# Performance work log

Measured on AMD Instinct MI355X. Metric: run time of the kernel, lower is better.

Reference implementation:

```python
import jax, jax.numpy as jnp
import numpy as np

B, T, U, V = 8, 128, 100, 1024
BLANK = 0
NEG = -1e30  # safe -inf surrogate (finite grads through logaddexp)


def setup_inputs() -> dict:
    key = jax.random.key(0)
    k1, k2 = jax.random.split(key)
    logits = jax.random.normal(k1, (B, T, U + 1, V), dtype=jnp.float32)
    # targets drawn from non-blank ids [1, V)
    targets = jax.random.randint(k2, (B, U), 1, V, dtype=jnp.int32)
    logit_lengths = jnp.full((B,), T, dtype=jnp.int32)
    target_lengths = jnp.full((B,), U, dtype=jnp.int32)
    return {"logits": logits, "targets": targets,
            "logit_lengths": logit_lengths, "target_lengths": target_lengths}


def _rnnt_nll(log_probs, targets, t_len, u_len):
    """Negative log-likelihood of one utterance.
    log_probs: [T, U+1, V] (log-softmaxed joiner output), targets: [U] int.
    alpha[t,u] = logaddexp(alpha[t-1,u] + blank[t-1,u], alpha[t,u-1] + emit[t,u-1]).
    """
    blank_lp = log_probs[:, :, BLANK]                      # [T, U+1]
    emit_lp = log_probs[:, jnp.arange(U), targets]         # [T, U]

    # row t=0: pure emissions
    alpha0 = jnp.concatenate([jnp.zeros((1,), log_probs.dtype),
                              jnp.cumsum(emit_lp[0])])     # [U+1]

    def combine(x, y):
        # linear log-space recurrence x[u] = logaddexp(c[u], x[u-1] + a[u])
        a1, c1 = x
        a2, c2 = y
        return (a1 + a2, jnp.logaddexp(c2, c1 + a2))

    def step(prev_row, inp):
        blank_prev, emit_t = inp                           # [U+1], [U]
        c = prev_row + blank_prev                          # vertical (blank) moves
        a = jnp.concatenate([jnp.full((1,), NEG, log_probs.dtype), emit_t])
        _, row = jax.lax.associative_scan(combine, (a, c))
        return row, row

    _, rows = jax.lax.scan(step, alpha0, (blank_lp[:-1], emit_lp[1:]))
    alpha = jnp.concatenate([alpha0[None, :], rows], axis=0)  # [T, U+1]

    ll = alpha[t_len - 1, u_len] + blank_lp[t_len - 1, u_len]
    return -ll


def reference(logits, targets, logit_lengths, target_lengths):
    log_probs = jax.nn.log_softmax(logits, axis=-1)
    # module passes src_lengths - 1 to rnnt_loss
    t_lens = logit_lengths - 1
    nll = jax.vmap(_rnnt_nll)(log_probs, targets, t_lens, target_lengths)
    return jnp.mean(nll)  # reduction='mean'
```

## Files before the change

kernel.cpp:

```cpp
#include <hip/hip_runtime.h>
#include <hip/hip_bf16.h>


constexpr int Bb = 8;
constexpr int Tt = 128;
constexpr int Uu = 100;
constexpr int Vv = 1024;
constexpr int UP1 = Uu + 1;
constexpr int DROWS = 244;
constexpr int DPAD  = 104;
constexpr int LROWS = 233;
constexpr int REG   = 29;
constexpr int NREG  = 8;

__device__ __forceinline__ unsigned short f2bf(float f) {
    unsigned int u = __builtin_bit_cast(unsigned int, f);
    u += 0x7fffu + ((u >> 16) & 1u);
    return (unsigned short)(u >> 16);
}
__device__ __forceinline__ float bflo(unsigned int p) {
    return __builtin_bit_cast(float, p << 16);
}
__device__ __forceinline__ float bfhi(unsigned int p) {
    return __builtin_bit_cast(float, p & 0xffff0000u);
}
__device__ __forceinline__ __hip_bfloat162 u2bf(unsigned int p) {
    __hip_bfloat162 h;
    __builtin_memcpy(&h, &p, sizeof(h));
    return h;
}
__device__ __forceinline__ unsigned int bf2u(__hip_bfloat162 h) {
    unsigned int p;
    __builtin_memcpy(&p, &h, sizeof(p));
    return p;
}

__device__ __forceinline__ unsigned int shr1u(unsigned int x) {
    return (unsigned int)__builtin_amdgcn_update_dpp(
        0, (int)x, 0x138, 0xf, 0xf, true);
}

__device__ __forceinline__ float readlane_f(float x, int lane) {
    return __builtin_bit_cast(float,
        __builtin_amdgcn_readlane(__builtin_bit_cast(int, x), lane));
}
__device__ __forceinline__ unsigned int readlane_u(unsigned int x, int lane) {
    return (unsigned int)__builtin_amdgcn_readlane((int)x, lane);
}

#define DPP_MAXSTEP(x, ctrl, rmask) {                                        \
    float _t = __builtin_bit_cast(float, __builtin_amdgcn_update_dpp(        \
        __builtin_bit_cast(int, x), __builtin_bit_cast(int, x),              \
        ctrl, rmask, 0xf, false));                                           \
    x = fmaxf(x, _t); }
#define WAVE_SCAN_MAX(x)           \
    DPP_MAXSTEP(x, 0x111, 0xf);    \
    DPP_MAXSTEP(x, 0x112, 0xf);    \
    DPP_MAXSTEP(x, 0x114, 0xf);    \
    DPP_MAXSTEP(x, 0x118, 0xf);    \
    DPP_MAXSTEP(x, 0x142, 0xa);    \
    DPP_MAXSTEP(x, 0x143, 0xc)

__global__ __launch_bounds__(256) void lse_kernel(
        const float* __restrict__ logits,
        const int*   __restrict__ targets,
        unsigned short* __restrict__ bS,
        unsigned short* __restrict__ eS,
        int* __restrict__ dcnt) {
    if (blockIdx.x == 0 && threadIdx.x == 0)
        __hip_atomic_store(dcnt, 0, __ATOMIC_RELAXED, __HIP_MEMORY_SCOPE_AGENT);

    const int wid  = blockIdx.x * 4 + (threadIdx.x >> 6);
    const int lane = threadIdx.x & 63;
    const int b   = wid / (Tt * UP1);
    const int rem = wid - b * (Tt * UP1);
    const int t   = rem / UP1;
    const int u   = rem - t * UP1;

    const float* row = logits + (size_t)wid * Vv;
    const float4* r4 = (const float4*)row;
    float4 x0 = r4[lane];
    float4 x1 = r4[lane + 64];
    float4 x2 = r4[lane + 128];
    float4 x3 = r4[lane + 192];

    float m = fmaxf(fmaxf(fmaxf(x0.x, x0.y), fmaxf(x0.z, x0.w)),
                    fmaxf(fmaxf(x1.x, x1.y), fmaxf(x1.z, x1.w)));
    m = fmaxf(m, fmaxf(fmaxf(fmaxf(x2.x, x2.y), fmaxf(x2.z, x2.w)),
                       fmaxf(fmaxf(x3.x, x3.y), fmaxf(x3.z, x3.w))));
    #pragma unroll
    for (int d = 32; d > 0; d >>= 1) m = fmaxf(m, __shfl_xor(m, d, 64));

    float s = __expf(x0.x - m) + __expf(x0.y - m) + __expf(x0.z - m) + __expf(x0.w - m)
            + __expf(x1.x - m) + __expf(x1.y - m) + __expf(x1.z - m) + __expf(x1.w - m)
            + __expf(x2.x - m) + __expf(x2.y - m) + __expf(x2.z - m) + __expf(x2.w - m)
            + __expf(x3.x - m) + __expf(x3.y - m) + __expf(x3.z - m) + __expf(x3.w - m);
    #pragma unroll
    for (int d = 32; d > 0; d >>= 1) s += __shfl_xor(s, d, 64);

    float lse = m + __logf(s);

    if (lane == 0) {
        const int dw = t + u + 1;
        bS[((size_t)b * DROWS + dw) * DPAD + u] = f2bf(__expf(x0.x - lse));
        if (u < Uu) {
            int tgt = targets[b * Uu + u];
            eS[((size_t)b * DROWS + dw) * DPAD + (u + 1)] = f2bf(__expf(row[tgt] - lse));
        }
    }
}

__global__ __launch_bounds__(576) void dp_kernel(
        const unsigned short* __restrict__ bS,
        const unsigned short* __restrict__ eS,
        const int* __restrict__ logit_lengths,
        const int* __restrict__ target_lengths,
        float* __restrict__ nll,
        int*   __restrict__ dcnt,
        float* __restrict__ out) {
    const int b    = blockIdx.x;
    const int tid  = threadIdx.x;
    const int wvi  = tid >> 6;
    const int lane = tid & 63;

    __shared__ __align__(16) unsigned short lB[LROWS][DPAD];
    __shared__ __align__(16) unsigned short lE[LROWS][DPAD];
    __shared__ int sflag[NREG];

    if (tid < NREG) sflag[tid] = 0;
    __syncthreads();

    const size_t bstride = (size_t)DROWS * DPAD;

    if (wvi >= 1) {
        const int w = wvi - 1;
        const int row0 = 1 + REG * w;
        constexpr int RBYTES = REG * DPAD * 2;
        const char* gb = (const char*)(bS + (size_t)b * bstride + (size_t)row0 * DPAD);
        const char* ge = (const char*)(eS + (size_t)b * bstride + (size_t)row0 * DPAD);
        char* db = (char*)&lB[row0][0];
        char* de = (char*)&lE[row0][0];
        for (int k = lane * 16; k < RBYTES; k += 64 * 16) {
            *(uint4*)(db + k) = *(const uint4*)(gb + k);
            *(uint4*)(de + k) = *(const uint4*)(ge + k);
        }
        if (lane < REG) {
            const int d = row0 + lane;
            lB[d][101] = 0; lB[d][102] = 0; lB[d][103] = 0;
            lE[d][0] = 0; lE[d][101] = 0; lE[d][102] = 0; lE[d][103] = 0;
        }
        __hip_atomic_store(&sflag[w], 1, __ATOMIC_RELEASE,
                           __HIP_MEMORY_SCOPE_WORKGROUP);
        return;
    }

    const int tl = logit_lengths[b];
    const int ul = target_lengths[b];
    const int t_idx = tl - 2;
    const int dcap  = t_idx + ul;

    const int u0 = lane * 2;

    unsigned int Pu = (lane == 0) ? 0x00003F80u : 0u;
    float S  = 0.0f;
    unsigned int capPu = (dcap == 0) ? 0x00003F80u : 0u;
    float capS = 0.0f;

#define PSTEP(dv, ubv, uev) do {                                       \
        unsigned int shP = shr1u(Pu);                                  \
        unsigned int M = __builtin_amdgcn_alignbit(Pu, shP, 16);       \
        Pu = bf2u(__hfma2(u2bf(ubv), u2bf(Pu),                         \
                          __hmul2(u2bf(uev), u2bf(M))));               \
        if ((dv) == dcap) { capPu = Pu; capS = S; }                    \
    } while (0)

#define RESCALE do {                                                   \
        float p0 = bflo(Pu), p1 = bfhi(Pu);                            \
        float gm = fmaxf(p0, p1);                                      \
        WAVE_SCAN_MAX(gm);                                             \
        float mm = fmaxf(readlane_f(gm, 63), 1e-30f);                  \
        float rr = 1.0f / mm;                                          \
        unsigned short rh = f2bf(rr);                                  \
        unsigned int rp = ((unsigned int)rh << 16) | rh;               \
        Pu = bf2u(__hmul2(u2bf(Pu), u2bf(rp)));                        \
        S += __logf(mm);                                               \
    } while (0)

#define LOADG(UB, UE, k) do {                                          \
        _Pragma("unroll")                                              \
        for (int r = 0; r < 8; ++r) {                                  \
            UB[r] = *(const unsigned int*)&lB[(k) * 8 + 1 + r][u0];    \
            UE[r] = *(const unsigned int*)&lE[(k) * 8 + 1 + r][u0];    \
        }                                                              \
    } while (0)

#define COMPG(UB, UE, k) do {                                          \
        _Pragma("unroll")                                              \
        for (int r = 0; r < 8; ++r)                                    \
            PSTEP((k) * 8 + 1 + r, UB[r], UE[r]);                      \
        RESCALE;                                                       \
    } while (0)

    int wcur = -1;
#define ENSURE(wn) do {                                                \
        while (wcur < (wn)) {                                          \
            ++wcur;                                                    \
            while (__hip_atomic_load(&sflag[wcur], __ATOMIC_ACQUIRE,   \
                       __HIP_MEMORY_SCOPE_WORKGROUP) == 0)             \
                __builtin_amdgcn_s_sleep(1);                           \
        }                                                              \
    } while (0)

    unsigned int Ab[8], Ae[8], Bb_[8], Be_[8];
    ENSURE(7 / REG);
    LOADG(Ab, Ae, 0);
    for (int c = 0; c < 14; ++c) {
        const int k0 = 2 * c, k1 = 2 * c + 1;
        ENSURE((8 * k1 + 7) / REG);
        LOADG(Bb_, Be_, k1);
        COMPG(Ab, Ae, k0);
        if (k1 < 28) {
            ENSURE((8 * (k1 + 1) + 7) / REG);
            LOADG(Ab, Ae, k1 + 1);
        }
        COMPG(Bb_, Be_, k1);
    }
    COMPG(Ab, Ae, 28);
#undef PSTEP
#undef RESCALE
#undef LOADG
#undef COMPG
#undef ENSURE

    unsigned int cw = readlane_u(capPu, ul >> 1);
    float capv = (ul & 1) ? bfhi(cw) : bflo(cw);

    if (lane == 0) {
        float blk = __builtin_bit_cast(float, ((unsigned int)lB[dcap + 1][ul]) << 16);
        float ll = __logf(capv) + capS + __logf(blk);
        __hip_atomic_store(&nll[b], -ll, __ATOMIC_RELEASE,
                           __HIP_MEMORY_SCOPE_AGENT);
        int prev = __hip_atomic_fetch_add(dcnt, 1, __ATOMIC_ACQ_REL,
                                          __HIP_MEMORY_SCOPE_AGENT);
        if (prev == Bb - 1) {
            float s = 0.0f;
            for (int i = 0; i < Bb; ++i)
                s += __hip_atomic_load(&nll[i], __ATOMIC_ACQUIRE,
                                       __HIP_MEMORY_SCOPE_AGENT);
            out[0] = s / (float)Bb;
        }
    }
}

extern "C" void kernel_launch(void* const* d_in, const int* in_sizes, int n_in,
                              void* d_out, int out_size, void* d_ws, size_t ws_size,
                              hipStream_t stream) {
    const float* logits         = (const float*)d_in[0];
    const int*   targets        = (const int*)d_in[1];
    const int*   logit_lengths  = (const int*)d_in[2];
    const int*   target_lengths = (const int*)d_in[3];
    float* out = (float*)d_out;

    int* dcnt = (int*)d_ws;
    unsigned short* bS = (unsigned short*)d_ws + 8;
    unsigned short* eS = bS + (size_t)Bb * DROWS * DPAD;
    float* nll = (float*)(eS + (size_t)Bb * DROWS * DPAD);

    const int rows = Bb * Tt * UP1;
    lse_kernel<<<rows / 4, 256, 0, stream>>>(logits, targets, bS, eS, dcnt);
    dp_kernel<<<Bb, 576, 0, stream>>>(bS, eS, logit_lengths, target_lengths,
                                      nll, dcnt, out);
}
```

Before: 97.06 us.

## Interleave blank/emit probabilities and run DP recurrence in fp32

Blank and emit probabilities now share one interleaved array, stored as pairs of (blank, emit) bf16 values per two columns, so each DP lane fetches both with one 8-byte LDS read. The staging waves use fully unrolled 16-byte copies with all loads issued before the stores. The anti-diagonal recurrence now keeps its state in fp32 registers with fma instead of packed bf16 arithmetic, which removes bf16 rounding from the accumulated state but roughly doubles the ALU ops per step on the serial critical path. The boundary zeroing is rewritten to match the new layout.

After: 88.81 us. 8.5% less time.

```diff
diff --git a/kernel.cpp b/kernel.cpp
--- a/kernel.cpp
+++ b/kernel.cpp
@@ -1,5 +1,4 @@
 #include <hip/hip_runtime.h>
-#include <hip/hip_bf16.h>
 
 
 constexpr int Bb = 8;
@@ -8,10 +7,12 @@
 constexpr int Vv = 1024;
 constexpr int UP1 = Uu + 1;
 constexpr int DROWS = 244;
-constexpr int DPAD  = 104;
+constexpr int PAIRS = 52;
+constexpr int ROWB  = PAIRS * 8;
 constexpr int LROWS = 233;
 constexpr int REG   = 29;
 constexpr int NREG  = 8;
+constexpr int RBYTES = REG * ROWB;
 
 __device__ __forceinline__ unsigned short f2bf(float f) {
     unsigned int u = __builtin_bit_cast(unsigned int, f);
@@ -24,28 +25,14 @@
 __device__ __forceinline__ float bfhi(unsigned int p) {
     return __builtin_bit_cast(float, p & 0xffff0000u);
 }
-__device__ __forceinline__ __hip_bfloat162 u2bf(unsigned int p) {
-    __hip_bfloat162 h;
-    __builtin_memcpy(&h, &p, sizeof(h));
-    return h;
-}
-__device__ __forceinline__ unsigned int bf2u(__hip_bfloat162 h) {
-    unsigned int p;
-    __builtin_memcpy(&p, &h, sizeof(p));
-    return p;
-}
-
-__device__ __forceinline__ unsigned int shr1u(unsigned int x) {
-    return (unsigned int)__builtin_amdgcn_update_dpp(
-        0, (int)x, 0x138, 0xf, 0xf, true);
-}
-
+
+__device__ __forceinline__ float wave_shr1(float x) {
+    return __builtin_bit_cast(float, __builtin_amdgcn_update_dpp(
+        0, __builtin_bit_cast(int, x), 0x138, 0xf, 0xf, true));
+}
 __device__ __forceinline__ float readlane_f(float x, int lane) {
     return __builtin_bit_cast(float,
         __builtin_amdgcn_readlane(__builtin_bit_cast(int, x), lane));
-}
-__device__ __forceinline__ unsigned int readlane_u(unsigned int x, int lane) {
-    return (unsigned int)__builtin_amdgcn_readlane((int)x, lane);
 }
 
 #define DPP_MAXSTEP(x, ctrl, rmask) {                                        \
@@ -64,8 +51,7 @@
 __global__ __launch_bounds__(256) void lse_kernel(
         const float* __restrict__ logits,
         const int*   __restrict__ targets,
-        unsigned short* __restrict__ bS,
-        unsigned short* __restrict__ eS,
+        unsigned short* __restrict__ gS,
         int* __restrict__ dcnt) {
     if (blockIdx.x == 0 && threadIdx.x == 0)
         __hip_atomic_store(dcnt, 0, __ATOMIC_RELAXED, __HIP_MEMORY_SCOPE_AGENT);
@@ -102,17 +88,18 @@
 
     if (lane == 0) {
         const int dw = t + u + 1;
-        bS[((size_t)b * DROWS + dw) * DPAD + u] = f2bf(__expf(x0.x - lse));
+        const size_t rowoff = ((size_t)b * DROWS + dw) * (PAIRS * 4);
+        gS[rowoff + (u >> 1) * 4 + (u & 1)] = f2bf(__expf(x0.x - lse));
         if (u < Uu) {
             int tgt = targets[b * Uu + u];
-            eS[((size_t)b * DROWS + dw) * DPAD + (u + 1)] = f2bf(__expf(row[tgt] - lse));
+            const int sidx = u + 1;
+            gS[rowoff + (sidx >> 1) * 4 + 2 + (sidx & 1)] = f2bf(__expf(row[tgt] - lse));
         }
     }
 }
 
 __global__ __launch_bounds__(576) void dp_kernel(
-        const unsigned short* __restrict__ bS,
-        const unsigned short* __restrict__ eS,
+        const unsigned short* __restrict__ gS,
         const int* __restrict__ logit_lengths,
         const int* __restrict__ target_lengths,
         float* __restrict__ nll,
@@ -123,31 +110,35 @@
     const int wvi  = tid >> 6;
     const int lane = tid & 63;
 
-    __shared__ __align__(16) unsigned short lB[LROWS][DPAD];
-    __shared__ __align__(16) unsigned short lE[LROWS][DPAD];
+    __shared__ __align__(16) unsigned short lBE[LROWS][PAIRS][4];
     __shared__ int sflag[NREG];
 
     if (tid < NREG) sflag[tid] = 0;
     __syncthreads();
-
-    const size_t bstride = (size_t)DROWS * DPAD;
 
     if (wvi >= 1) {
         const int w = wvi - 1;
         const int row0 = 1 + REG * w;
-        constexpr int RBYTES = REG * DPAD * 2;
-        const char* gb = (const char*)(bS + (size_t)b * bstride + (size_t)row0 * DPAD);
-        const char* ge = (const char*)(eS + (size_t)b * bstride + (size_t)row0 * DPAD);
-        char* db = (char*)&lB[row0][0];
-        char* de = (char*)&lE[row0][0];
-        for (int k = lane * 16; k < RBYTES; k += 64 * 16) {
-            *(uint4*)(db + k) = *(const uint4*)(gb + k);
-            *(uint4*)(de + k) = *(const uint4*)(ge + k);
-        }
+        const char* gb = (const char*)gS + ((size_t)b * DROWS + row0) * ROWB;
+        char* db = (char*)lBE + (size_t)row0 * ROWB;
+
+        uint4 v[12];
+        #pragma unroll
+        for (int i = 0; i < 12; ++i)
+            v[i] = *(const uint4*)(gb + lane * 16 + i * 1024);
+        #pragma unroll
+        for (int i = 0; i < 11; ++i)
+            *(uint4*)(db + lane * 16 + i * 1024) = v[i];
+        if (lane < 50)
+            *(uint4*)(db + lane * 16 + 11 * 1024) = v[11];
+
         if (lane < REG) {
             const int d = row0 + lane;
-            lB[d][101] = 0; lB[d][102] = 0; lB[d][103] = 0;
-            lE[d][0] = 0; lE[d][101] = 0; lE[d][102] = 0; lE[d][103] = 0;
+            lBE[d][0][2]  = 0;
+            lBE[d][50][1] = 0;
+            lBE[d][50][3] = 0;
+            lBE[d][51][0] = 0; lBE[d][51][1] = 0;
+            lBE[d][51][2] = 0; lBE[d][51][3] = 0;
         }
         __hip_atomic_store(&sflag[w], 1, __ATOMIC_RELEASE,
                            __HIP_MEMORY_SCOPE_WORKGROUP);
@@ -159,38 +150,39 @@
     const int t_idx = tl - 2;
     const int dcap  = t_idx + ul;
 
-    const int u0 = lane * 2;
-
-    unsigned int Pu = (lane == 0) ? 0x00003F80u : 0u;
+    const int lpair = (lane < 51) ? lane : 51;
+    const char* lbase = (const char*)lBE + lpair * 8;
+
+    float P0 = (lane == 0) ? 1.0f : 0.0f;
+    float P1 = 0.0f;
     float S  = 0.0f;
-    unsigned int capPu = (dcap == 0) ? 0x00003F80u : 0u;
-    float capS = 0.0f;
-
-#define PSTEP(dv, ubv, uev) do {                                       \
-        unsigned int shP = shr1u(Pu);                                  \
-        unsigned int M = __builtin_amdgcn_alignbit(Pu, shP, 16);       \
-        Pu = bf2u(__hfma2(u2bf(ubv), u2bf(Pu),                         \
-                          __hmul2(u2bf(uev), u2bf(M))));               \
-        if ((dv) == dcap) { capPu = Pu; capS = S; }                    \
+    float capP0 = (dcap == 0) ? 1.0f : 0.0f, capP1 = 0.0f, capS = 0.0f;
+
+#define PSTEP(dv, w0, w1) do {                                         \
+        float Bx = bflo(w0), By = bfhi(w0);                            \
+        float Ex = bflo(w1), Ey = bfhi(w1);                            \
+        float sh = wave_shr1(P1);                                      \
+        float n1 = fmaf(P1, By, P0 * Ey);                              \
+        float n0 = fmaf(P0, Bx, sh * Ex);                              \
+        P0 = n0; P1 = n1;                                              \
+        if ((dv) == dcap) { capP0 = n0; capP1 = n1; capS = S; }        \
     } while (0)
 
 #define RESCALE do {                                                   \
-        float p0 = bflo(Pu), p1 = bfhi(Pu);                            \
-        float gm = fmaxf(p0, p1);                                      \
+        float gm = fmaxf(P0, P1);                                      \
         WAVE_SCAN_MAX(gm);                                             \
         float mm = fmaxf(readlane_f(gm, 63), 1e-30f);                  \
         float rr = 1.0f / mm;                                          \
-        unsigned short rh = f2bf(rr);                                  \
-        unsigned int rp = ((unsigned int)rh << 16) | rh;               \
-        Pu = bf2u(__hmul2(u2bf(Pu), u2bf(rp)));                        \
+        P0 *= rr; P1 *= rr;                                            \
         S += __logf(mm);                                               \
     } while (0)
 
 #define LOADG(UB, UE, k) do {                                          \
         _Pragma("unroll")                                              \
         for (int r = 0; r < 8; ++r) {                                  \
-            UB[r] = *(const unsigned int*)&lB[(k) * 8 + 1 + r][u0];    \
-            UE[r] = *(const unsigned int*)&lE[(k) * 8 + 1 + r][u0];    \
+            uint2 q = *(const uint2*)(lbase +                          \
+                        (size_t)((k) * 8 + 1 + r) * ROWB);             \
+            UB[r] = q.x; UE[r] = q.y;                                  \
         }                                                              \
     } while (0)
 
@@ -212,7 +204,7 @@
     } while (0)
 
     unsigned int Ab[8], Ae[8], Bb_[8], Be_[8];
-    ENSURE(7 / REG);
+    ENSURE(0);
     LOADG(Ab, Ae, 0);
     for (int c = 0; c < 14; ++c) {
         const int k0 = 2 * c, k1 = 2 * c + 1;
@@ -232,11 +224,13 @@
 #undef COMPG
 #undef ENSURE
 
-    unsigned int cw = readlane_u(capPu, ul >> 1);
-    float capv = (ul & 1) ? bfhi(cw) : bflo(cw);
+    float w0 = readlane_f(capP0, ul >> 1);
+    float w1 = readlane_f(capP1, ul >> 1);
+    float capv = (ul & 1) ? w1 : w0;
 
     if (lane == 0) {
-        float blk = __builtin_bit_cast(float, ((unsigned int)lB[dcap + 1][ul]) << 16);
+        unsigned short hv = lBE[dcap + 1][ul >> 1][ul & 1];
+        float blk = __builtin_bit_cast(float, ((unsigned int)hv) << 16);
         float ll = __logf(capv) + capS + __logf(blk);
         __hip_atomic_store(&nll[b], -ll, __ATOMIC_RELEASE,
                            __HIP_MEMORY_SCOPE_AGENT);
@@ -262,12 +256,11 @@
     float* out = (float*)d_out;
 
     int* dcnt = (int*)d_ws;
-    unsigned short* bS = (unsigned short*)d_ws + 8;
-    unsigned short* eS = bS + (size_t)Bb * DROWS * DPAD;
-    float* nll = (float*)(eS + (size_t)Bb * DROWS * DPAD);
+    unsigned short* gS = (unsigned short*)d_ws + 16;
+    float* nll = (float*)(gS + (size_t)Bb * DROWS * PAIRS * 4);
 
     const int rows = Bb * Tt * UP1;
-    lse_kernel<<<rows / 4, 256, 0, stream>>>(logits, targets, bS, eS, dcnt);
-    dp_kernel<<<Bb, 576, 0, stream>>>(bS, eS, logit_lengths, target_lengths,
+    lse_kernel<<<rows / 4, 256, 0, stream>>>(logits, targets, gS, dcnt);
+    dp_kernel<<<Bb, 576, 0, stream>>>(gS, logit_lengths, target_lengths,
                                       nll, dcnt, out);
 }
```
